# Optimization experiments

Hardware: AMD Instinct MI355X
Metric: run time of the kernel (lower is better)

## Reference

```python
import jax, jax.numpy as jnp
import numpy as np

H = 64  # hidden width hard-coded in Agent body


def setup_inputs() -> dict:
    key = jax.random.key(0)
    ks = jax.random.split(key, 10)
    T, B, OBS, A = 1024, 512, 128, 18
    x = jax.random.normal(ks[0], (T, B, OBS), dtype=jnp.float32)
    mask = jax.random.bernoulli(ks[1], 0.01, (T, B))
    initial_carry = jnp.zeros((B, H), dtype=jnp.float32)
    s = lambda k, sh: (jax.random.normal(k, sh, dtype=jnp.float32) * 0.05)
    W1 = s(ks[2], (OBS, H)); b1 = jnp.zeros((H,), jnp.float32)
    Wi = s(ks[3], (H, 3 * H)); bi = jnp.zeros((3 * H,), jnp.float32)
    Wh = s(ks[4], (H, 3 * H)); bhn = jnp.zeros((H,), jnp.float32)
    W2 = s(ks[5], (H, H)); b2 = jnp.zeros((H,), jnp.float32)
    Wl = s(ks[6], (H, A)); bl = jnp.zeros((A,), jnp.float32)
    Wv = s(ks[7], (H, 1)); bv = jnp.zeros((1,), jnp.float32)
    return dict(x=x, mask=mask, initial_carry=initial_carry,
                W1=W1, b1=b1, Wi=Wi, bi=bi, Wh=Wh, bhn=bhn,
                W2=W2, b2=b2, Wl=Wl, bl=bl, Wv=Wv, bv=bv)


def _gru(h, z_t, Wi, bi, Wh, bhn):
    # flax nn.GRUCell math
    gi = z_t @ Wi + bi            # [B, 3H]
    gh = h @ Wh                   # [B, 3H]
    ir, iz, inn = jnp.split(gi, 3, axis=-1)
    hr, hz, hn = jnp.split(gh, 3, axis=-1)
    r = jax.nn.sigmoid(ir + hr)
    u = jax.nn.sigmoid(iz + hz)
    n = jnp.tanh(inn + r * (hn + bhn))
    return (1.0 - u) * n + u * h


def reference(x, mask, initial_carry, W1, b1, Wi, bi, Wh, bhn, W2, b2, Wl, bl, Wv, bv):
    # stem: Dense(64) + relu, applied to all timesteps at once
    z = jax.nn.relu(x @ W1 + b1)                  # [T, B, H]
    m = mask[..., None]                           # [T, B, 1]

    def step(h, inp):
        z_t, m_t = inp
        # masked reset of the carry at episode boundaries
        h = jnp.where(m_t, initial_carry, h)
        h = _gru(h, z_t, Wi, bi, Wh, bhn)
        return h, h

    h_final, ys = jax.lax.scan(step, initial_carry, (z, m))  # ys: [T, B, H]

    y = jax.nn.relu(ys @ W2 + b2)                 # [T, B, H]
    logits = y @ Wl + bl                          # [T, B, A]
    value = y @ Wv + bv                           # [T, B, 1]
    return h_final, logits.squeeze(), value.squeeze(-1)
```

## Files before the change

kernel.cpp:

```cpp
#include <hip/hip_runtime.h>
#include <stdint.h>

#define TT  1024
#define BB  512
#define OBS 128
#define HH  64
#define AA  18
#define RT  (TT*BB)
#define OFF_L ((size_t)BB*HH)
#define OFF_V (OFF_L + (size_t)TT*BB*AA)

#define GI_ELEMS ((size_t)RT*192)
#define WS_NEED  ((GI_ELEMS + (size_t)RT*HH)*4)

typedef __attribute__((ext_vector_type(8))) short bf16x8;
typedef __attribute__((ext_vector_type(4))) float f32x4;
typedef __attribute__((ext_vector_type(4))) unsigned int u32x4;

__device__ __forceinline__ float fast_rcp(float x){ return __builtin_amdgcn_rcpf(x); }
__device__ __forceinline__ float sigm(float x){ return fast_rcp(1.f + __expf(-x)); }
__device__ __forceinline__ float tanh_(float x){ return 1.f - 2.f*fast_rcp(1.f + __expf(2.f*x)); }

__device__ __forceinline__ unsigned bf16_rne(float f){
    unsigned u = __float_as_uint(f);
    return (u + 0x7FFFu + ((u>>16)&1u)) >> 16;
}
__device__ __forceinline__ unsigned pk_bf16(float lo, float hi){
    unsigned d;
    asm("v_cvt_pk_bf16_f32 %0, %1, %2" : "=v"(d) : "v"(lo), "v"(hi));
    return d;
}

__global__ void detect_mask(const uint32_t* __restrict__ m, uint32_t* __restrict__ flag)
{
    const int n_words = (TT * BB) / 4;
    uint32_t acc = 0;
    for (int i = blockIdx.x * blockDim.x + threadIdx.x; i < n_words;
         i += gridDim.x * blockDim.x)
        acc |= (m[i] > 1u) ? 1u : 0u;
    if (acc) flag[0] = 1u;
}

#define P1_BLOCKS 1024
#define ZSTR 70

__global__ __launch_bounds__(256, 2)
void stem_gi(const float* __restrict__ x,
             const float* __restrict__ W1, const float* __restrict__ b1,
             const float* __restrict__ Wi, const float* __restrict__ bi,
             float* __restrict__ gi)
{
    const int tid = threadIdx.x, w = tid >> 6, l = tid & 63;
    const int a = l & 15, q = l >> 4;

    __shared__ float z_s[4][16*ZSTR];
    float* zw = &z_s[w][0];

    bf16x8 W1f[4][4];
    #pragma unroll
    for (int nt = 0; nt < 4; ++nt)
        #pragma unroll
        for (int kf = 0; kf < 4; ++kf) {
            u32x4 pk;
            #pragma unroll
            for (int j2 = 0; j2 < 4; ++j2) {
                const int k0 = kf*32 + q*8 + 2*j2;
                pk[j2] = bf16_rne(W1[(size_t)k0*HH + nt*16 + a])
                       | (bf16_rne(W1[(size_t)(k0+1)*HH + nt*16 + a]) << 16);
            }
            W1f[nt][kf] = __builtin_bit_cast(bf16x8, pk);
        }
    float b1v[4];
    #pragma unroll
    for (int nt = 0; nt < 4; ++nt) b1v[nt] = b1[nt*16 + a];

    bf16x8 Wif[12][2];
    #pragma unroll
    for (int tau = 0; tau < 12; ++tau)
        #pragma unroll
        for (int kf = 0; kf < 2; ++kf) {
            u32x4 pk;
            #pragma unroll
            for (int j2 = 0; j2 < 4; ++j2) {
                const int k0 = kf*32 + q*8 + 2*j2;
                pk[j2] = bf16_rne(Wi[(size_t)k0*192 + tau*16 + a])
                       | (bf16_rne(Wi[(size_t)(k0+1)*192 + tau*16 + a]) << 16);
            }
            Wif[tau][kf] = __builtin_bit_cast(bf16x8, pk);
        }
    float biv[12];
    #pragma unroll
    for (int tau = 0; tau < 12; ++tau) biv[tau] = bi[tau*16 + a];

    for (int it = 0; it < 8; ++it) {
        const size_t grp  = (size_t)blockIdx.x*32 + it*4 + w;
        const float* xr   = x + (grp*16 + a)*OBS;

        float4 xv[8];
        #pragma unroll
        for (int kf = 0; kf < 4; ++kf) {
            xv[2*kf]   = *(const float4*)(xr + kf*32 + q*8);
            xv[2*kf+1] = *(const float4*)(xr + kf*32 + q*8 + 4);
        }
        bf16x8 Af[4];
        #pragma unroll
        for (int kf = 0; kf < 4; ++kf) {
            u32x4 pk;
            pk[0] = pk_bf16(xv[2*kf].x,   xv[2*kf].y);
            pk[1] = pk_bf16(xv[2*kf].z,   xv[2*kf].w);
            pk[2] = pk_bf16(xv[2*kf+1].x, xv[2*kf+1].y);
            pk[3] = pk_bf16(xv[2*kf+1].z, xv[2*kf+1].w);
            Af[kf] = __builtin_bit_cast(bf16x8, pk);
        }

        #pragma unroll
        for (int nt = 0; nt < 4; ++nt) {
            f32x4 D = {b1v[nt], b1v[nt], b1v[nt], b1v[nt]};
            #pragma unroll
            for (int kf = 0; kf < 4; ++kf)
                D = __builtin_amdgcn_mfma_f32_16x16x32_bf16(Af[kf], W1f[nt][kf], D, 0,0,0);
            #pragma unroll
            for (int e = 0; e < 4; ++e)
                zw[(q*4 + e)*ZSTR + nt*16 + a] = fmaxf(D[e], 0.f);
        }
        bf16x8 Az[2];
        #pragma unroll
        for (int s = 0; s < 2; ++s) {
            u32x4 pk;
            #pragma unroll
            for (int j2 = 0; j2 < 4; ++j2) {
                const float2 f = *(const float2*)(zw + a*ZSTR + s*32 + q*8 + 2*j2);
                pk[j2] = pk_bf16(f.x, f.y);
            }
            Az[s] = __builtin_bit_cast(bf16x8, pk);
        }

        float* gb = gi + grp*12*256 + l*4;
        #pragma unroll
        for (int tau = 0; tau < 12; ++tau) {
            f32x4 D = {biv[tau], biv[tau], biv[tau], biv[tau]};
            D = __builtin_amdgcn_mfma_f32_16x16x32_bf16(Az[0], Wif[tau][0], D, 0,0,0);
            D = __builtin_amdgcn_mfma_f32_16x16x32_bf16(Az[1], Wif[tau][1], D, 0,0,0);
            *(f32x4*)(gb + (size_t)tau*256) = D;
        }
    }
}

__global__ __launch_bounds__(256)
void recur5(const float* __restrict__ gip,
            const void* __restrict__ mask_raw,
            const uint32_t* __restrict__ mflag,
            const float* __restrict__ ic,
            const float* __restrict__ Wh,
            const float* __restrict__ bhn,
            float* __restrict__ ys,
            float* __restrict__ out)
{
    const int blk = blockIdx.x;
    const int tid = threadIdx.x;
    const int w   = tid >> 6;
    const int l   = tid & 63;
    const int a   = l & 15;
    const int q   = l >> 4;
    const int dw  = w*16 + a;

    __shared__ float    h_lds[2][64][17];
    __shared__ uint32_t mbits[TT];

    if (mflag[0] != 0) {
        const uint8_t* m8 = (const uint8_t*)mask_raw;
        for (int t0 = w*4; t0 < TT; t0 += 16) {
            const int tt = t0 + q;
            const uint64_t bal = __ballot(m8[(size_t)tt*BB + blk*16 + a] != 0);
            if (l < 4) mbits[t0 + l] = (uint32_t)((bal >> (16*l)) & 0xFFFFu);
        }
    } else {
        const int32_t* m32 = (const int32_t*)mask_raw;
        for (int t0 = w*4; t0 < TT; t0 += 16) {
            const int tt = t0 + q;
            const uint64_t bal = __ballot(m32[(size_t)tt*BB + blk*16 + a] != 0);
            if (l < 4) mbits[t0 + l] = (uint32_t)((bal >> (16*l)) & 0xFFFFu);
        }
    }
    for (int i = tid; i < 16*64; i += 256) {
        const int c = i & 15, d = i >> 4;
        h_lds[0][d][c] = ic[(blk*16 + c)*HH + d];
    }

    bf16x8 Bf[3][2];
    #pragma unroll
    for (int g = 0; g < 3; ++g) {
        const int colb = g*64 + dw;
        #pragma unroll
        for (int s = 0; s < 2; ++s) {
            u32x4 pk;
            #pragma unroll
            for (int j2 = 0; j2 < 4; ++j2) {
                const int k0 = s*32 + q*8 + j2*2;
                pk[j2] = bf16_rne(Wh[(size_t)k0*192 + colb])
                       | (bf16_rne(Wh[(size_t)(k0+1)*192 + colb]) << 16);
            }
            Bf[g][s] = __builtin_bit_cast(bf16x8, pk);
        }
    }
    u32x4 icA[2];
    #pragma unroll
    for (int s = 0; s < 2; ++s) {
        #pragma unroll
        for (int j2 = 0; j2 < 4; ++j2) {
            const int d0 = s*32 + q*8 + j2*2;
            icA[s][j2] = bf16_rne(ic[(blk*16 + a)*HH + d0])
                       | (bf16_rne(ic[(blk*16 + a)*HH + d0 + 1]) << 16);
        }
    }
    float ic_c[4], h_reg[4];
    #pragma unroll
    for (int e = 0; e < 4; ++e) {
        ic_c[e]  = ic[(blk*16 + q*4 + e)*HH + dw];
        h_reg[e] = ic_c[e];
    }
    const float bhnv = bhn[dw];
    const f32x4 Cn = {bhnv, bhnv, bhnv, bhnv};

    __syncthreads();

    #define GSTRIDE ((size_t)32*12*256)
    const float* gbase = gip + (size_t)blk*12*256 + l*4;
    f32x4 bufA[3], bufB[3];
    #pragma unroll
    for (int g = 0; g < 3; ++g) {
        bufA[g] = *(const f32x4*)(gbase + 0*GSTRIDE + (size_t)(g*4 + w)*256);
        bufB[g] = *(const f32x4*)(gbase + 1*GSTRIDE + (size_t)(g*4 + w)*256);
    }

    auto step = [&](int t, f32x4* cur) {
        const int p = t & 1;
        const uint32_t mb = mbits[t];
        const bool mA = (mb >> a) & 1;
        u32x4 Apk[2];
        #pragma unroll
        for (int s = 0; s < 2; ++s) {
            #pragma unroll
            for (int j2 = 0; j2 < 4; ++j2) {
                const int d0 = s*32 + q*8 + j2*2;
                const unsigned pkv = pk_bf16(h_lds[p][d0][a], h_lds[p][d0+1][a]);
                Apk[s][j2] = mA ? icA[s][j2] : pkv;
            }
        }
        const bf16x8 A0 = __builtin_bit_cast(bf16x8, Apk[0]);
        const bf16x8 A1 = __builtin_bit_cast(bf16x8, Apk[1]);
        f32x4 Dr = __builtin_amdgcn_mfma_f32_16x16x32_bf16(A0, Bf[0][0], cur[0], 0,0,0);
        Dr       = __builtin_amdgcn_mfma_f32_16x16x32_bf16(A1, Bf[0][1], Dr,     0,0,0);
        f32x4 Dz = __builtin_amdgcn_mfma_f32_16x16x32_bf16(A0, Bf[1][0], cur[1], 0,0,0);
        Dz       = __builtin_amdgcn_mfma_f32_16x16x32_bf16(A1, Bf[1][1], Dz,     0,0,0);
        f32x4 Dn = __builtin_amdgcn_mfma_f32_16x16x32_bf16(A0, Bf[2][0], Cn,     0,0,0);
        Dn       = __builtin_amdgcn_mfma_f32_16x16x32_bf16(A1, Bf[2][1], Dn,     0,0,0);
        const f32x4 gin = cur[2];
        const int tp = (t + 2 < TT) ? (t + 2) : (TT - 1);
        #pragma unroll
        for (int g = 0; g < 3; ++g)
            cur[g] = *(const f32x4*)(gbase + (size_t)tp*GSTRIDE + (size_t)(g*4 + w)*256);
        float* ysp = ys + ((size_t)t*BB + blk*16 + q*4)*HH + dw;
        #pragma unroll
        for (int e = 0; e < 4; ++e) {
            const bool me   = (mb >> (q*4 + e)) & 1;
            const float he  = me ? ic_c[e] : h_reg[e];
            const float r   = sigm(Dr[e]);
            const float u   = sigm(Dz[e]);
            const float n   = tanh_(fmaf(r, Dn[e], gin[e]));
            const float hn  = fmaf(u, he - n, n);
            h_reg[e] = hn;
            h_lds[p ^ 1][dw][q*4 + e] = hn;
            ysp[(size_t)e*HH] = hn;
        }
        __syncthreads();
    };

    for (int t = 0; t < TT; t += 2) {
        step(t,     bufA);
        step(t + 1, bufB);
    }
    #pragma unroll
    for (int e = 0; e < 4; ++e)
        out[(size_t)(blk*16 + q*4 + e)*HH + dw] = h_reg[e];
    #undef GSTRIDE
}

#define P3_BLOCKS 1024
#define P3_RPW (RT/(P3_BLOCKS*4))

__global__ __launch_bounds__(256, 2)
void heads(const float* __restrict__ ys,
           const float* __restrict__ W2, const float* __restrict__ b2,
           const float* __restrict__ Wl, const float* __restrict__ bl,
           const float* __restrict__ Wv, const float* __restrict__ bv,
           float* __restrict__ out)
{
    const int tid = threadIdx.x, w = tid >> 6, lane = tid & 63;
    __shared__ float4 sb[4][2][16];
    float w2r[64];
    #pragma unroll
    for (int k = 0; k < 64; ++k) w2r[k] = W2[k*HH + lane];
    const float b2v = b2[lane];
    float wc[64]; float bcv = 0.f;
    if (lane < AA) {
        #pragma unroll
        for (int k = 0; k < 64; ++k) wc[k] = Wl[k*AA + lane];
        bcv = bl[lane];
    } else if (lane == AA) {
        #pragma unroll
        for (int k = 0; k < 64; ++k) wc[k] = Wv[k];
        bcv = bv[0];
    } else {
        #pragma unroll
        for (int k = 0; k < 64; ++k) wc[k] = 0.f;
    }
    const int r0 = (blockIdx.x*4 + w) * P3_RPW;
    float ysA = ys[(size_t)r0*HH + lane];
    float ysB = ys[(size_t)(r0+1)*HH + lane];
    for (int rr = 0; rr < P3_RPW; ++rr) {
        const int row = r0 + rr;
        const float ysv = ysA;
        ysA = ysB;
        const int rn = (rr+2 < P3_RPW) ? (row+2) : (r0 + P3_RPW - 1);
        ysB = ys[(size_t)rn*HH + lane];
        ((float*)&sb[w][0][0])[lane] = ysv;
        float acc = b2v;
        {
            const float4* yb = &sb[w][0][0];
            #pragma unroll
            for (int kk = 0; kk < 16; ++kk) {
                const float4 v = yb[kk];
                acc += w2r[4*kk+0]*v.x + w2r[4*kk+1]*v.y
                     + w2r[4*kk+2]*v.z + w2r[4*kk+3]*v.w;
            }
        }
        const float yv = fmaxf(acc, 0.f);
        ((float*)&sb[w][1][0])[lane] = yv;
        float acc2 = bcv;
        {
            const float4* yb = &sb[w][1][0];
            #pragma unroll
            for (int kk = 0; kk < 16; ++kk) {
                const float4 v = yb[kk];
                acc2 += wc[4*kk+0]*v.x + wc[4*kk+1]*v.y
                      + wc[4*kk+2]*v.z + wc[4*kk+3]*v.w;
            }
        }
        if (lane < AA)       out[OFF_L + (size_t)row*AA + lane] = acc2;
        else if (lane == AA) out[OFF_V + row] = acc2;
    }
}

__global__ __launch_bounds__(256, 2)
void gru_agent(const float* __restrict__ x,
               const void* __restrict__ mask_raw,
               const uint32_t* __restrict__ mask_flag,
               const float* __restrict__ ic,
               const float* __restrict__ W1, const float* __restrict__ b1,
               const float* __restrict__ Wi, const float* __restrict__ bi,
               const float* __restrict__ Wh, const float* __restrict__ bhn,
               const float* __restrict__ W2, const float* __restrict__ b2,
               const float* __restrict__ Wl, const float* __restrict__ bl,
               const float* __restrict__ Wv, const float* __restrict__ bv,
               float* __restrict__ out)
{
    const int b    = blockIdx.x;
    const int tid  = threadIdx.x;
    const int w    = tid >> 6;
    const int lane = tid & 63;

    const bool mask_is_u8 = (mask_flag[0] != 0);
    const uint8_t* __restrict__ m8  = (const uint8_t*)mask_raw;
    const int32_t* __restrict__ m32 = (const int32_t*)mask_raw;

    __shared__ float4 x_l[2][4][9];
    __shared__ float4 z_l[16];
    __shared__ float4 h_l[2][16];
    __shared__ float4 y_l[2][16];
    __shared__ float4 ic_l[16];
    __shared__ float  gi_l[192];
    __shared__ float  gh_l[192];

    const int js = (w << 4) | (lane >> 2);
    const int kc = lane & 3;
    float w1r[32];
    #pragma unroll
    for (int i = 0; i < 32; ++i) w1r[i] = W1[(kc*32 + i)*HH + js];
    const float b1v = b1[js];

    float wA[64], wB[64];
    float biv = 0.f, b2v = 0.f, blv = 0.f;
    if (w < 3) {
        const int n = tid;
        #pragma unroll
        for (int k = 0; k < 64; ++k) wA[k] = Wi[k*(3*HH) + n];
        #pragma unroll
        for (int k = 0; k < 64; ++k) wB[k] = Wh[k*(3*HH) + n];
        biv = bi[n];
    } else {
        #pragma unroll
        for (int k = 0; k < 64; ++k) wA[k] = W2[k*HH + lane];
        #pragma unroll
        for (int k = 0; k < 64; ++k) wB[k] = (lane < AA) ? Wl[k*AA + lane]
                                           : (lane == AA ? Wv[k] : 0.f);
        b2v = b2[lane];
        blv = (lane < AA) ? bl[lane] : (lane == AA ? bv[0] : 0.f);
    }
    const float bhnv = (tid < HH) ? bhn[tid] : 0.f;

    if (tid < HH) {
        float v = ic[b*HH + tid];
        ((float*)ic_l)[tid]   = v;
        ((float*)h_l[0])[tid] = v;
    }
    if (tid < OBS) {
        float xv = x[(0*BB + b)*OBS + tid];
        ((float*)&x_l[0][tid>>5])[tid&31] = xv;
    }
    uint8_t m_cur = mask_is_u8 ? m8[b] : (uint8_t)(m32[b] != 0);
    __syncthreads();

    for (int t = 0; t < TT + 2; ++t) {
        const int p = t & 1;
        float xnext = 0.f;
        if (t + 1 < TT && tid < OBS) xnext = x[((t+1)*BB + b)*OBS + tid];
        uint8_t m_next = 0;
        if (t + 1 < TT) {
            const int mi = (t+1)*BB + b;
            m_next = mask_is_u8 ? m8[mi] : (uint8_t)(m32[mi] != 0);
        }
        if (t < TT) {
            const float4* xr = &x_l[p][kc][0];
            float acc = 0.f;
            #pragma unroll
            for (int qq = 0; qq < 8; ++qq) {
                float4 xv = xr[qq];
                acc += w1r[4*qq+0]*xv.x + w1r[4*qq+1]*xv.y
                     + w1r[4*qq+2]*xv.z + w1r[4*qq+3]*xv.w;
            }
            acc += __shfl_xor(acc, 1);
            acc += __shfl_xor(acc, 2);
            if (kc == 0) ((float*)z_l)[js] = fmaxf(acc + b1v, 0.f);
        }
        if (t < TT && w < 3) {
            const float4* hs = m_cur ? ic_l : h_l[p];
            float acc = 0.f;
            #pragma unroll
            for (int kk = 0; kk < 16; ++kk) {
                float4 hv = hs[kk];
                acc += wB[4*kk+0]*hv.x + wB[4*kk+1]*hv.y
                     + wB[4*kk+2]*hv.z + wB[4*kk+3]*hv.w;
            }
            gh_l[tid] = acc;
        } else if (w == 3 && t >= 1 && t <= TT) {
            const float4* hs = h_l[p];
            float acc = b2v;
            #pragma unroll
            for (int kk = 0; kk < 16; ++kk) {
                float4 hv = hs[kk];
                acc += wA[4*kk+0]*hv.x + wA[4*kk+1]*hv.y
                     + wA[4*kk+2]*hv.z + wA[4*kk+3]*hv.w;
            }
            ((float*)y_l[p])[lane] = fmaxf(acc, 0.f);
        }
        __syncthreads();
        if (t < TT && w < 3) {
            float acc = biv;
            #pragma unroll
            for (int kk = 0; kk < 16; ++kk) {
                float4 zv = z_l[kk];
                acc += wA[4*kk+0]*zv.x + wA[4*kk+1]*zv.y
                     + wA[4*kk+2]*zv.z + wA[4*kk+3]*zv.w;
            }
            gi_l[tid] = acc;
        } else if (w == 3 && t >= 2) {
            const float4* yss = y_l[p ^ 1];
            float acc = blv;
            #pragma unroll
            for (int kk = 0; kk < 16; ++kk) {
                float4 yv = yss[kk];
                acc += wB[4*kk+0]*yv.x + wB[4*kk+1]*yv.y
                     + wB[4*kk+2]*yv.z + wB[4*kk+3]*yv.w;
            }
            if (lane < AA)       out[OFF_L + (size_t)((t-2)*BB + b)*AA + lane] = acc;
            else if (lane == AA) out[OFF_V + (size_t)(t-2)*BB + b] = acc;
        }
        __syncthreads();
        if (t < TT && tid < HH) {
            const int j = tid;
            const float irv = gi_l[j], izv = gi_l[HH+j], inn = gi_l[2*HH+j];
            const float hrv = gh_l[j], hzv = gh_l[HH+j], hnv = gh_l[2*HH+j];
            const float heff = m_cur ? ((const float*)ic_l)[j]
                                     : ((const float*)h_l[p])[j];
            const float r  = sigm(irv + hrv);
            const float u  = sigm(izv + hzv);
            const float nn = tanh_(inn + r*(hnv + bhnv));
            ((float*)h_l[p ^ 1])[j] = u*(heff - nn) + nn;
        }
        if (t + 1 < TT && tid < OBS) {
            ((float*)&x_l[p ^ 1][tid>>5])[tid&31] = xnext;
        }
        m_cur = m_next;
        __syncthreads();
    }
    if (tid < HH) out[(size_t)b*HH + tid] = ((const float*)h_l[TT & 1])[tid];
}

extern "C" void kernel_launch(void* const* d_in, const int* in_sizes, int n_in,
                              void* d_out, int out_size, void* d_ws, size_t ws_size,
                              hipStream_t stream) {
    const float* x    = (const float*)d_in[0];
    const void*  mask = (const void*) d_in[1];
    const float* ic   = (const float*)d_in[2];
    const float* W1   = (const float*)d_in[3];
    const float* b1   = (const float*)d_in[4];
    const float* Wi   = (const float*)d_in[5];
    const float* bi   = (const float*)d_in[6];
    const float* Wh   = (const float*)d_in[7];
    const float* bhn  = (const float*)d_in[8];
    const float* W2   = (const float*)d_in[9];
    const float* b2   = (const float*)d_in[10];
    const float* Wl   = (const float*)d_in[11];
    const float* bl   = (const float*)d_in[12];
    const float* Wv   = (const float*)d_in[13];
    const float* bv   = (const float*)d_in[14];
    float* out = (float*)d_out;

    if (ws_size >= WS_NEED) {
        float* gi = (float*)d_ws;
        float* ys = gi + GI_ELEMS;
        uint32_t* flag = (uint32_t*)(out + OFF_V + RT - 1);
        hipMemsetAsync(flag, 0, sizeof(uint32_t), stream);
        detect_mask<<<64, 256, 0, stream>>>((const uint32_t*)mask, flag);
        stem_gi<<<P1_BLOCKS, 256, 0, stream>>>(x, W1, b1, Wi, bi, gi);
        recur5<<<32, 256, 0, stream>>>(gi, mask, flag, ic, Wh, bhn, ys, out);
        heads<<<P3_BLOCKS, 256, 0, stream>>>(ys, W2, b2, Wl, bl, Wv, bv, out);
    } else {
        uint32_t* flag = (uint32_t*)d_ws;
        hipMemsetAsync(flag, 0, sizeof(uint32_t), stream);
        detect_mask<<<64, 256, 0, stream>>>((const uint32_t*)mask, flag);
        gru_agent<<<BB, 256, 0, stream>>>(x, mask, flag, ic, W1, b1, Wi, bi, Wh, bhn,
                                          W2, b2, Wl, bl, Wv, bv, out);
    }
}
```

Before: 1.088 ms.

## Fuse output heads into the recurrent kernel using MFMA on the LDS state

Drops the separate heads kernel and the ys workspace round-trip. The recurrent kernel now computes relu(h@W2+b2) with MFMA each step from the bf16-packed hidden state in LDS, stores it in a second LDS buffer, and runs the logits/value MFMA one step behind on two of the four waves. This removes writing and re-reading the full [T,B,64] sequence through global memory and one kernel launch. The cost is extra MFMA and LDS work on the latency-bound serial recurrence that only 32 blocks execute, and the head matmuls now run in bf16 instead of fp32.

```diff
diff --git a/kernel.cpp b/kernel.cpp
--- a/kernel.cpp
+++ b/kernel.cpp
@@ -147,13 +147,15 @@
 }
 
 __global__ __launch_bounds__(256)
-void recur5(const float* __restrict__ gip,
+void recur7(const float* __restrict__ gip,
             const void* __restrict__ mask_raw,
             const uint32_t* __restrict__ mflag,
             const float* __restrict__ ic,
             const float* __restrict__ Wh,
             const float* __restrict__ bhn,
-            float* __restrict__ ys,
+            const float* __restrict__ W2, const float* __restrict__ b2,
+            const float* __restrict__ Wl, const float* __restrict__ bl,
+            const float* __restrict__ Wv, const float* __restrict__ bv,
             float* __restrict__ out)
 {
     const int blk = blockIdx.x;
@@ -165,6 +167,7 @@
     const int dw  = w*16 + a;
 
     __shared__ float    h_lds[2][64][17];
+    __shared__ float    y_lds[2][64][17];
     __shared__ uint32_t mbits[TT];
 
     if (mflag[0] != 0) {
@@ -203,16 +206,57 @@
             Bf[g][s] = __builtin_bit_cast(bf16x8, pk);
         }
     }
+    bf16x8 W2f[2];
+    #pragma unroll
+    for (int s = 0; s < 2; ++s) {
+        u32x4 pk;
+        #pragma unroll
+        for (int j2 = 0; j2 < 4; ++j2) {
+            const int k0 = s*32 + q*8 + j2*2;
+            pk[j2] = bf16_rne(W2[(size_t)k0*HH + dw])
+                   | (bf16_rne(W2[(size_t)(k0+1)*HH + dw]) << 16);
+        }
+        W2f[s] = __builtin_bit_cast(bf16x8, pk);
+    }
+    const float b2v = b2[dw];
+    bf16x8 Wlf[2];
+    float blv = 0.f;
+    {
+        #pragma unroll
+        for (int s = 0; s < 2; ++s) {
+            u32x4 pk;
+            #pragma unroll
+            for (int j2 = 0; j2 < 4; ++j2) {
+                const int k0 = s*32 + q*8 + j2*2;
+                unsigned lo = 0, hi = 0;
+                if (w == 0) {
+                    lo = bf16_rne(Wl[(size_t)k0*AA + a]);
+                    hi = bf16_rne(Wl[(size_t)(k0+1)*AA + a]);
+                } else if (w == 1) {
+                    if (a < 2) {
+                        lo = bf16_rne(Wl[(size_t)k0*AA + 16 + a]);
+                        hi = bf16_rne(Wl[(size_t)(k0+1)*AA + 16 + a]);
+                    } else if (a == 2) {
+                        lo = bf16_rne(Wv[k0]);
+                        hi = bf16_rne(Wv[k0+1]);
+                    }
+                }
+                pk[j2] = lo | (hi << 16);
+            }
+            Wlf[s] = __builtin_bit_cast(bf16x8, pk);
+        }
+        if (w == 0)      blv = bl[a];
+        else if (w == 1) blv = (a < 2) ? bl[16 + a] : (a == 2 ? bv[0] : 0.f);
+    }
     u32x4 icA[2];
     #pragma unroll
-    for (int s = 0; s < 2; ++s) {
+    for (int s = 0; s < 2; ++s)
         #pragma unroll
         for (int j2 = 0; j2 < 4; ++j2) {
             const int d0 = s*32 + q*8 + j2*2;
             icA[s][j2] = bf16_rne(ic[(blk*16 + a)*HH + d0])
                        | (bf16_rne(ic[(blk*16 + a)*HH + d0 + 1]) << 16);
         }
-    }
     float ic_c[4], h_reg[4];
     #pragma unroll
     for (int e = 0; e < 4; ++e) {
@@ -232,35 +276,70 @@
         bufA[g] = *(const f32x4*)(gbase + 0*GSTRIDE + (size_t)(g*4 + w)*256);
         bufB[g] = *(const f32x4*)(gbase + 1*GSTRIDE + (size_t)(g*4 + w)*256);
     }
+
+    auto do_logits = [&](int pp, int row_t) {
+        u32x4 Y0, Y1;
+        #pragma unroll
+        for (int j2 = 0; j2 < 4; ++j2) {
+            const int d0 = q*8 + j2*2;
+            Y0[j2] = pk_bf16(y_lds[pp][d0][a],      y_lds[pp][d0+1][a]);
+            Y1[j2] = pk_bf16(y_lds[pp][32+d0][a],   y_lds[pp][32+d0+1][a]);
+        }
+        f32x4 Dl = {blv, blv, blv, blv};
+        Dl = __builtin_amdgcn_mfma_f32_16x16x32_bf16(
+                 __builtin_bit_cast(bf16x8, Y0), Wlf[0], Dl, 0,0,0);
+        Dl = __builtin_amdgcn_mfma_f32_16x16x32_bf16(
+                 __builtin_bit_cast(bf16x8, Y1), Wlf[1], Dl, 0,0,0);
+        if (w == 0) {
+            #pragma unroll
+            for (int e = 0; e < 4; ++e)
+                out[OFF_L + ((size_t)row_t*BB + blk*16 + q*4 + e)*AA + a] = Dl[e];
+        } else {
+            if (a < 2) {
+                #pragma unroll
+                for (int e = 0; e < 4; ++e)
+                    out[OFF_L + ((size_t)row_t*BB + blk*16 + q*4 + e)*AA + 16 + a] = Dl[e];
+            } else if (a == 2) {
+                #pragma unroll
+                for (int e = 0; e < 4; ++e)
+                    out[OFF_V + (size_t)row_t*BB + blk*16 + q*4 + e] = Dl[e];
+            }
+        }
+    };
 
     auto step = [&](int t, f32x4* cur) {
         const int p = t & 1;
         const uint32_t mb = mbits[t];
         const bool mA = (mb >> a) & 1;
-        u32x4 Apk[2];
-        #pragma unroll
-        for (int s = 0; s < 2; ++s) {
-            #pragma unroll
-            for (int j2 = 0; j2 < 4; ++j2) {
-                const int d0 = s*32 + q*8 + j2*2;
-                const unsigned pkv = pk_bf16(h_lds[p][d0][a], h_lds[p][d0+1][a]);
-                Apk[s][j2] = mA ? icA[s][j2] : pkv;
-            }
-        }
-        const bf16x8 A0 = __builtin_bit_cast(bf16x8, Apk[0]);
-        const bf16x8 A1 = __builtin_bit_cast(bf16x8, Apk[1]);
+        u32x4 Araw0, Araw1, Apk0, Apk1;
+        #pragma unroll
+        for (int j2 = 0; j2 < 4; ++j2) {
+            const int d0 = q*8 + j2*2;
+            const unsigned r0 = pk_bf16(h_lds[p][d0][a],      h_lds[p][d0+1][a]);
+            const unsigned r1 = pk_bf16(h_lds[p][32+d0][a],   h_lds[p][32+d0+1][a]);
+            Araw0[j2] = r0;             Araw1[j2] = r1;
+            Apk0[j2]  = mA ? icA[0][j2] : r0;
+            Apk1[j2]  = mA ? icA[1][j2] : r1;
+        }
+        const bf16x8 A0  = __builtin_bit_cast(bf16x8, Apk0);
+        const bf16x8 A1  = __builtin_bit_cast(bf16x8, Apk1);
+        const bf16x8 Ar0 = __builtin_bit_cast(bf16x8, Araw0);
+        const bf16x8 Ar1 = __builtin_bit_cast(bf16x8, Araw1);
         f32x4 Dr = __builtin_amdgcn_mfma_f32_16x16x32_bf16(A0, Bf[0][0], cur[0], 0,0,0);
         Dr       = __builtin_amdgcn_mfma_f32_16x16x32_bf16(A1, Bf[0][1], Dr,     0,0,0);
         f32x4 Dz = __builtin_amdgcn_mfma_f32_16x16x32_bf16(A0, Bf[1][0], cur[1], 0,0,0);
         Dz       = __builtin_amdgcn_mfma_f32_16x16x32_bf16(A1, Bf[1][1], Dz,     0,0,0);
         f32x4 Dn = __builtin_amdgcn_mfma_f32_16x16x32_bf16(A0, Bf[2][0], Cn,     0,0,0);
         Dn       = __builtin_amdgcn_mfma_f32_16x16x32_bf16(A1, Bf[2][1], Dn,     0,0,0);
+        f32x4 Dy = {b2v, b2v, b2v, b2v};
+        Dy = __builtin_amdgcn_mfma_f32_16x16x32_bf16(Ar0, W2f[0], Dy, 0,0,0);
+        Dy = __builtin_amdgcn_mfma_f32_16x16x32_bf16(Ar1, W2f[1], Dy, 0,0,0);
+        if (w < 2 && t >= 2) do_logits(p, t - 2);
         const f32x4 gin = cur[2];
         const int tp = (t + 2 < TT) ? (t + 2) : (TT - 1);
         #pragma unroll
         for (int g = 0; g < 3; ++g)
             cur[g] = *(const f32x4*)(gbase + (size_t)tp*GSTRIDE + (size_t)(g*4 + w)*256);
-        float* ysp = ys + ((size_t)t*BB + blk*16 + q*4)*HH + dw;
         #pragma unroll
         for (int e = 0; e < 4; ++e) {
             const bool me   = (mb >> (q*4 + e)) & 1;
@@ -271,7 +350,7 @@
             const float hn  = fmaf(u, he - n, n);
             h_reg[e] = hn;
             h_lds[p ^ 1][dw][q*4 + e] = hn;
-            ysp[(size_t)e*HH] = hn;
+            y_lds[p ^ 1][dw][q*4 + e] = fmaxf(Dy[e], 0.f);
         }
         __syncthreads();
     };
@@ -280,76 +359,32 @@
         step(t,     bufA);
         step(t + 1, bufB);
     }
+
+    {
+        const int p = TT & 1;
+        u32x4 Araw0, Araw1;
+        #pragma unroll
+        for (int j2 = 0; j2 < 4; ++j2) {
+            const int d0 = q*8 + j2*2;
+            Araw0[j2] = pk_bf16(h_lds[p][d0][a],    h_lds[p][d0+1][a]);
+            Araw1[j2] = pk_bf16(h_lds[p][32+d0][a], h_lds[p][32+d0+1][a]);
+        }
+        f32x4 Dy = {b2v, b2v, b2v, b2v};
+        Dy = __builtin_amdgcn_mfma_f32_16x16x32_bf16(
+                 __builtin_bit_cast(bf16x8, Araw0), W2f[0], Dy, 0,0,0);
+        Dy = __builtin_amdgcn_mfma_f32_16x16x32_bf16(
+                 __builtin_bit_cast(bf16x8, Araw1), W2f[1], Dy, 0,0,0);
+        if (w < 2) do_logits(p, TT - 2);
+        #pragma unroll
+        for (int e = 0; e < 4; ++e)
+            y_lds[p ^ 1][dw][q*4 + e] = fmaxf(Dy[e], 0.f);
+        __syncthreads();
+        if (w < 2) do_logits(p ^ 1, TT - 1);
+    }
     #pragma unroll
     for (int e = 0; e < 4; ++e)
         out[(size_t)(blk*16 + q*4 + e)*HH + dw] = h_reg[e];
     #undef GSTRIDE
-}
-
-#define P3_BLOCKS 1024
-#define P3_RPW (RT/(P3_BLOCKS*4))
-
-__global__ __launch_bounds__(256, 2)
-void heads(const float* __restrict__ ys,
-           const float* __restrict__ W2, const float* __restrict__ b2,
-           const float* __restrict__ Wl, const float* __restrict__ bl,
-           const float* __restrict__ Wv, const float* __restrict__ bv,
-           float* __restrict__ out)
-{
-    const int tid = threadIdx.x, w = tid >> 6, lane = tid & 63;
-    __shared__ float4 sb[4][2][16];
-    float w2r[64];
-    #pragma unroll
-    for (int k = 0; k < 64; ++k) w2r[k] = W2[k*HH + lane];
-    const float b2v = b2[lane];
-    float wc[64]; float bcv = 0.f;
-    if (lane < AA) {
-        #pragma unroll
-        for (int k = 0; k < 64; ++k) wc[k] = Wl[k*AA + lane];
-        bcv = bl[lane];
-    } else if (lane == AA) {
-        #pragma unroll
-        for (int k = 0; k < 64; ++k) wc[k] = Wv[k];
-        bcv = bv[0];
-    } else {
-        #pragma unroll
-        for (int k = 0; k < 64; ++k) wc[k] = 0.f;
-    }
-    const int r0 = (blockIdx.x*4 + w) * P3_RPW;
-    float ysA = ys[(size_t)r0*HH + lane];
-    float ysB = ys[(size_t)(r0+1)*HH + lane];
-    for (int rr = 0; rr < P3_RPW; ++rr) {
-        const int row = r0 + rr;
-        const float ysv = ysA;
-        ysA = ysB;
-        const int rn = (rr+2 < P3_RPW) ? (row+2) : (r0 + P3_RPW - 1);
-        ysB = ys[(size_t)rn*HH + lane];
-        ((float*)&sb[w][0][0])[lane] = ysv;
-        float acc = b2v;
-        {
-            const float4* yb = &sb[w][0][0];
-            #pragma unroll
-            for (int kk = 0; kk < 16; ++kk) {
-                const float4 v = yb[kk];
-                acc += w2r[4*kk+0]*v.x + w2r[4*kk+1]*v.y
-                     + w2r[4*kk+2]*v.z + w2r[4*kk+3]*v.w;
-            }
-        }
-        const float yv = fmaxf(acc, 0.f);
-        ((float*)&sb[w][1][0])[lane] = yv;
-        float acc2 = bcv;
-        {
-            const float4* yb = &sb[w][1][0];
-            #pragma unroll
-            for (int kk = 0; kk < 16; ++kk) {
-                const float4 v = yb[kk];
-                acc2 += wc[4*kk+0]*v.x + wc[4*kk+1]*v.y
-                      + wc[4*kk+2]*v.z + wc[4*kk+3]*v.w;
-            }
-        }
-        if (lane < AA)       out[OFF_L + (size_t)row*AA + lane] = acc2;
-        else if (lane == AA) out[OFF_V + row] = acc2;
-    }
 }
 
 __global__ __launch_bounds__(256, 2)
@@ -529,13 +564,12 @@
 
     if (ws_size >= WS_NEED) {
         float* gi = (float*)d_ws;
-        float* ys = gi + GI_ELEMS;
-        uint32_t* flag = (uint32_t*)(out + OFF_V + RT - 1);
+        uint32_t* flag = (uint32_t*)(gi + GI_ELEMS);
         hipMemsetAsync(flag, 0, sizeof(uint32_t), stream);
         detect_mask<<<64, 256, 0, stream>>>((const uint32_t*)mask, flag);
         stem_gi<<<P1_BLOCKS, 256, 0, stream>>>(x, W1, b1, Wi, bi, gi);
-        recur5<<<32, 256, 0, stream>>>(gi, mask, flag, ic, Wh, bhn, ys, out);
-        heads<<<P3_BLOCKS, 256, 0, stream>>>(ys, W2, b2, Wl, bl, Wv, bv, out);
+        recur7<<<32, 256, 0, stream>>>(gi, mask, flag, ic, Wh, bhn,
+                                       W2, b2, Wl, bl, Wv, bv, out);
     } else {
         uint32_t* flag = (uint32_t*)d_ws;
         hipMemsetAsync(flag, 0, sizeof(uint32_t), stream);
```

Result: slower. 1.343 ms (+23.4%).

## Process two 16-row batch groups per recurrence block to interleave independent chains

Applied to the files above, without the earlier changes.

The recurrent kernel now handles 32 batch rows per block as two independent 16-row groups, launching 16 blocks instead of 32. The two groups' MFMA chains, gate math and loads are interleaved within each timestep, so one group's latency can hide behind the other's work and both share a single barrier per step. The cost is half as many blocks in flight on a large GPU, more registers and LDS per block, and longer per-step instruction streams. Because the recurrence is latency bound, the per-step critical path may lengthen instead of overlapping.

```diff
diff --git a/kernel.cpp b/kernel.cpp
--- a/kernel.cpp
+++ b/kernel.cpp
@@ -147,7 +147,7 @@
 }
 
 __global__ __launch_bounds__(256)
-void recur5(const float* __restrict__ gip,
+void recur8(const float* __restrict__ gip,
             const void* __restrict__ mask_raw,
             const uint32_t* __restrict__ mflag,
             const float* __restrict__ ic,
@@ -164,27 +164,34 @@
     const int q   = l >> 4;
     const int dw  = w*16 + a;
 
-    __shared__ float    h_lds[2][64][17];
-    __shared__ uint32_t mbits[TT];
+    __shared__ float    h_lds[2][2][64][17];
+    __shared__ uint32_t mbits[2][TT];
 
     if (mflag[0] != 0) {
         const uint8_t* m8 = (const uint8_t*)mask_raw;
-        for (int t0 = w*4; t0 < TT; t0 += 16) {
-            const int tt = t0 + q;
-            const uint64_t bal = __ballot(m8[(size_t)tt*BB + blk*16 + a] != 0);
-            if (l < 4) mbits[t0 + l] = (uint32_t)((bal >> (16*l)) & 0xFFFFu);
-        }
+        #pragma unroll
+        for (int G = 0; G < 2; ++G)
+            for (int t0 = w*4; t0 < TT; t0 += 16) {
+                const int tt = t0 + q;
+                const uint64_t bal =
+                    __ballot(m8[(size_t)tt*BB + blk*32 + G*16 + a] != 0);
+                if (l < 4) mbits[G][t0 + l] = (uint32_t)((bal >> (16*l)) & 0xFFFFu);
+            }
     } else {
         const int32_t* m32 = (const int32_t*)mask_raw;
-        for (int t0 = w*4; t0 < TT; t0 += 16) {
-            const int tt = t0 + q;
-            const uint64_t bal = __ballot(m32[(size_t)tt*BB + blk*16 + a] != 0);
-            if (l < 4) mbits[t0 + l] = (uint32_t)((bal >> (16*l)) & 0xFFFFu);
-        }
-    }
-    for (int i = tid; i < 16*64; i += 256) {
-        const int c = i & 15, d = i >> 4;
-        h_lds[0][d][c] = ic[(blk*16 + c)*HH + d];
+        #pragma unroll
+        for (int G = 0; G < 2; ++G)
+            for (int t0 = w*4; t0 < TT; t0 += 16) {
+                const int tt = t0 + q;
+                const uint64_t bal =
+                    __ballot(m32[(size_t)tt*BB + blk*32 + G*16 + a] != 0);
+                if (l < 4) mbits[G][t0 + l] = (uint32_t)((bal >> (16*l)) & 0xFFFFu);
+            }
+    }
+    for (int i = tid; i < 2*16*64; i += 256) {
+        const int G = i >> 10, j = i & 1023;
+        const int c = j & 15, d = j >> 4;
+        h_lds[G][0][d][c] = ic[(blk*32 + G*16 + c)*HH + d];
     }
 
     bf16x8 Bf[3][2];
@@ -203,75 +210,95 @@
             Bf[g][s] = __builtin_bit_cast(bf16x8, pk);
         }
     }
-    u32x4 icA[2];
-    #pragma unroll
-    for (int s = 0; s < 2; ++s) {
-        #pragma unroll
-        for (int j2 = 0; j2 < 4; ++j2) {
-            const int d0 = s*32 + q*8 + j2*2;
-            icA[s][j2] = bf16_rne(ic[(blk*16 + a)*HH + d0])
-                       | (bf16_rne(ic[(blk*16 + a)*HH + d0 + 1]) << 16);
-        }
-    }
-    float ic_c[4], h_reg[4];
-    #pragma unroll
-    for (int e = 0; e < 4; ++e) {
-        ic_c[e]  = ic[(blk*16 + q*4 + e)*HH + dw];
-        h_reg[e] = ic_c[e];
-    }
+    u32x4 icA[2][2];
+    #pragma unroll
+    for (int G = 0; G < 2; ++G)
+        #pragma unroll
+        for (int s = 0; s < 2; ++s)
+            #pragma unroll
+            for (int j2 = 0; j2 < 4; ++j2) {
+                const int d0 = s*32 + q*8 + j2*2;
+                icA[G][s][j2] = bf16_rne(ic[(blk*32 + G*16 + a)*HH + d0])
+                              | (bf16_rne(ic[(blk*32 + G*16 + a)*HH + d0 + 1]) << 16);
+            }
+    float ic_c[2][4], h_reg[2][4];
+    #pragma unroll
+    for (int G = 0; G < 2; ++G)
+        #pragma unroll
+        for (int e = 0; e < 4; ++e) {
+            ic_c[G][e]  = ic[(blk*32 + G*16 + q*4 + e)*HH + dw];
+            h_reg[G][e] = ic_c[G][e];
+        }
     const float bhnv = bhn[dw];
     const f32x4 Cn = {bhnv, bhnv, bhnv, bhnv};
 
     __syncthreads();
 
     #define GSTRIDE ((size_t)32*12*256)
-    const float* gbase = gip + (size_t)blk*12*256 + l*4;
-    f32x4 bufA[3], bufB[3];
+    const float* gbase0 = gip + (size_t)(blk*2 + 0)*12*256 + l*4;
+    const float* gbase1 = gip + (size_t)(blk*2 + 1)*12*256 + l*4;
+    f32x4 bufA[2][3], bufB[2][3];
     #pragma unroll
     for (int g = 0; g < 3; ++g) {
-        bufA[g] = *(const f32x4*)(gbase + 0*GSTRIDE + (size_t)(g*4 + w)*256);
-        bufB[g] = *(const f32x4*)(gbase + 1*GSTRIDE + (size_t)(g*4 + w)*256);
-    }
-
-    auto step = [&](int t, f32x4* cur) {
+        bufA[0][g] = *(const f32x4*)(gbase0 + 0*GSTRIDE + (size_t)(g*4 + w)*256);
+        bufA[1][g] = *(const f32x4*)(gbase1 + 0*GSTRIDE + (size_t)(g*4 + w)*256);
+        bufB[0][g] = *(const f32x4*)(gbase0 + 1*GSTRIDE + (size_t)(g*4 + w)*256);
+        bufB[1][g] = *(const f32x4*)(gbase1 + 1*GSTRIDE + (size_t)(g*4 + w)*256);
+    }
+
+    auto step = [&](int t, f32x4 (&cur)[2][3]) {
         const int p = t & 1;
-        const uint32_t mb = mbits[t];
-        const bool mA = (mb >> a) & 1;
-        u32x4 Apk[2];
-        #pragma unroll
-        for (int s = 0; s < 2; ++s) {
+        const int tp = (t + 2 < TT) ? (t + 2) : (TT - 1);
+        bf16x8 A0[2], A1[2];
+        uint32_t mbv[2];
+        #pragma unroll
+        for (int G = 0; G < 2; ++G) {
+            const uint32_t mb = mbits[G][t];
+            mbv[G] = mb;
+            const bool mA = (mb >> a) & 1;
+            u32x4 Apk0, Apk1;
             #pragma unroll
             for (int j2 = 0; j2 < 4; ++j2) {
-                const int d0 = s*32 + q*8 + j2*2;
-                const unsigned pkv = pk_bf16(h_lds[p][d0][a], h_lds[p][d0+1][a]);
-                Apk[s][j2] = mA ? icA[s][j2] : pkv;
-            }
-        }
-        const bf16x8 A0 = __builtin_bit_cast(bf16x8, Apk[0]);
-        const bf16x8 A1 = __builtin_bit_cast(bf16x8, Apk[1]);
-        f32x4 Dr = __builtin_amdgcn_mfma_f32_16x16x32_bf16(A0, Bf[0][0], cur[0], 0,0,0);
-        Dr       = __builtin_amdgcn_mfma_f32_16x16x32_bf16(A1, Bf[0][1], Dr,     0,0,0);
-        f32x4 Dz = __builtin_amdgcn_mfma_f32_16x16x32_bf16(A0, Bf[1][0], cur[1], 0,0,0);
-        Dz       = __builtin_amdgcn_mfma_f32_16x16x32_bf16(A1, Bf[1][1], Dz,     0,0,0);
-        f32x4 Dn = __builtin_amdgcn_mfma_f32_16x16x32_bf16(A0, Bf[2][0], Cn,     0,0,0);
-        Dn       = __builtin_amdgcn_mfma_f32_16x16x32_bf16(A1, Bf[2][1], Dn,     0,0,0);
-        const f32x4 gin = cur[2];
-        const int tp = (t + 2 < TT) ? (t + 2) : (TT - 1);
-        #pragma unroll
-        for (int g = 0; g < 3; ++g)
-            cur[g] = *(const f32x4*)(gbase + (size_t)tp*GSTRIDE + (size_t)(g*4 + w)*256);
-        float* ysp = ys + ((size_t)t*BB + blk*16 + q*4)*HH + dw;
-        #pragma unroll
-        for (int e = 0; e < 4; ++e) {
-            const bool me   = (mb >> (q*4 + e)) & 1;
-            const float he  = me ? ic_c[e] : h_reg[e];
-            const float r   = sigm(Dr[e]);
-            const float u   = sigm(Dz[e]);
-            const float n   = tanh_(fmaf(r, Dn[e], gin[e]));
-            const float hn  = fmaf(u, he - n, n);
-            h_reg[e] = hn;
-            h_lds[p ^ 1][dw][q*4 + e] = hn;
-            ysp[(size_t)e*HH] = hn;
+                const int d0 = q*8 + j2*2;
+                const unsigned r0 = pk_bf16(h_lds[G][p][d0][a],    h_lds[G][p][d0+1][a]);
+                const unsigned r1 = pk_bf16(h_lds[G][p][32+d0][a], h_lds[G][p][32+d0+1][a]);
+                Apk0[j2] = mA ? icA[G][0][j2] : r0;
+                Apk1[j2] = mA ? icA[G][1][j2] : r1;
+            }
+            A0[G] = __builtin_bit_cast(bf16x8, Apk0);
+            A1[G] = __builtin_bit_cast(bf16x8, Apk1);
+        }
+        f32x4 Dr[2], Dz[2], Dn[2], gin[2];
+        #pragma unroll
+        for (int G = 0; G < 2; ++G) {
+            Dr[G] = __builtin_amdgcn_mfma_f32_16x16x32_bf16(A0[G], Bf[0][0], cur[G][0], 0,0,0);
+            Dr[G] = __builtin_amdgcn_mfma_f32_16x16x32_bf16(A1[G], Bf[0][1], Dr[G],     0,0,0);
+            Dz[G] = __builtin_amdgcn_mfma_f32_16x16x32_bf16(A0[G], Bf[1][0], cur[G][1], 0,0,0);
+            Dz[G] = __builtin_amdgcn_mfma_f32_16x16x32_bf16(A1[G], Bf[1][1], Dz[G],     0,0,0);
+            Dn[G] = __builtin_amdgcn_mfma_f32_16x16x32_bf16(A0[G], Bf[2][0], Cn,        0,0,0);
+            Dn[G] = __builtin_amdgcn_mfma_f32_16x16x32_bf16(A1[G], Bf[2][1], Dn[G],     0,0,0);
+            gin[G] = cur[G][2];
+        }
+        #pragma unroll
+        for (int g = 0; g < 3; ++g) {
+            cur[0][g] = *(const f32x4*)(gbase0 + (size_t)tp*GSTRIDE + (size_t)(g*4 + w)*256);
+            cur[1][g] = *(const f32x4*)(gbase1 + (size_t)tp*GSTRIDE + (size_t)(g*4 + w)*256);
+        }
+        #pragma unroll
+        for (int G = 0; G < 2; ++G) {
+            float* ysp = ys + ((size_t)t*BB + blk*32 + G*16 + q*4)*HH + dw;
+            #pragma unroll
+            for (int e = 0; e < 4; ++e) {
+                const bool me   = (mbv[G] >> (q*4 + e)) & 1;
+                const float he  = me ? ic_c[G][e] : h_reg[G][e];
+                const float r   = sigm(Dr[G][e]);
+                const float u   = sigm(Dz[G][e]);
+                const float n   = tanh_(fmaf(r, Dn[G][e], gin[G][e]));
+                const float hn  = fmaf(u, he - n, n);
+                h_reg[G][e] = hn;
+                h_lds[G][p ^ 1][dw][q*4 + e] = hn;
+                ysp[(size_t)e*HH] = hn;
+            }
         }
         __syncthreads();
     };
@@ -281,8 +308,10 @@
         step(t + 1, bufB);
     }
     #pragma unroll
-    for (int e = 0; e < 4; ++e)
-        out[(size_t)(blk*16 + q*4 + e)*HH + dw] = h_reg[e];
+    for (int G = 0; G < 2; ++G)
+        #pragma unroll
+        for (int e = 0; e < 4; ++e)
+            out[(size_t)(blk*32 + G*16 + q*4 + e)*HH + dw] = h_reg[G][e];
     #undef GSTRIDE
 }
 
@@ -534,7 +563,7 @@
         hipMemsetAsync(flag, 0, sizeof(uint32_t), stream);
         detect_mask<<<64, 256, 0, stream>>>((const uint32_t*)mask, flag);
         stem_gi<<<P1_BLOCKS, 256, 0, stream>>>(x, W1, b1, Wi, bi, gi);
-        recur5<<<32, 256, 0, stream>>>(gi, mask, flag, ic, Wh, bhn, ys, out);
+        recur8<<<16, 256, 0, stream>>>(gi, mask, flag, ic, Wh, bhn, ys, out);
         heads<<<P3_BLOCKS, 256, 0, stream>>>(ys, W2, b2, Wl, bl, Wv, bv, out);
     } else {
         uint32_t* flag = (uint32_t*)d_ws;
```

New measurement: 1.448 ms. 33.0% more time.
